# Optimization experiments

Hardware: AMD Instinct MI355X
Metric: run time of the kernel (lower is better)

Reference implementation:

```python
import jax, jax.numpy as jnp
import numpy as np

N_NODES = 100000
N_EDGES = 4800000


def gcn_conv(x, edge_index, W, b):
    """PyG GCNConv: add self-loops, symmetric deg^-1/2 normalization, scatter-add."""
    n = x.shape[0]
    loops = jnp.arange(n, dtype=edge_index.dtype)
    src = jnp.concatenate([edge_index[0], loops])  # [E+N] message sources
    dst = jnp.concatenate([edge_index[1], loops])  # [E+N] message targets
    deg = jax.ops.segment_sum(jnp.ones_like(dst, dtype=x.dtype), dst, num_segments=n)
    dinv = jnp.where(deg > 0, jax.lax.rsqrt(deg), 0.0)  # deg^{-1/2}, guard isolated nodes
    norm = dinv[src] * dinv[dst]                  # [E+N]
    h = x @ W                                      # [N, out] tiny GEMM
    msg = h[src] * norm[:, None]                   # gather + scale (memory bound)
    out = jax.ops.segment_sum(msg, dst, num_segments=n)  # scatter-add
    return out + b


def setup_inputs() -> dict:
    key = jax.random.key(0)
    k1, k2, k3, k4 = jax.random.split(key, 4)
    node_features = jax.random.normal(k1, (N_NODES, 1), dtype=jnp.float32)
    edge_index = jax.random.randint(k2, (2, N_EDGES), 0, N_NODES, dtype=jnp.int32)
    W1 = jax.random.normal(k3, (1, 16), dtype=jnp.float32) / jnp.sqrt(1.0)
    b1 = jnp.zeros((16,), dtype=jnp.float32)
    W2 = jax.random.normal(k4, (16, 2), dtype=jnp.float32) / jnp.sqrt(16.0)
    b2 = jnp.zeros((2,), dtype=jnp.float32)
    return {"node_features": node_features, "edge_index": edge_index,
            "W1": W1, "b1": b1, "W2": W2, "b2": b2}


def reference(node_features, edge_index, W1, b1, W2, b2):
    h = gcn_conv(node_features, edge_index, W1, b1)
    h = jax.nn.relu(h)
    h = gcn_conv(h, edge_index, W2, b2)
    return jax.nn.log_softmax(h, axis=1)
```

## Files before the change

### kernel.cpp

```cpp
#include <hip/hip_runtime.h>
#include <math.h>


#define NNODES 100000
#define NEDGES 4800000
#define BN 256
#define NB 391
#define NPAD (NB * BN)
#define B1 512
#define CHUNK 9375
#define SEG 4
#define SRC_BITS 17
#define SRC_MASK 0x1FFFF

__global__ __launch_bounds__(512) void hist_k(const int* __restrict__ dst,
                                              int* __restrict__ blockhist, int E) {
    __shared__ int h[NB];
    int blk = blockIdx.x;
    for (int i = threadIdx.x; i < NB; i += 512) h[i] = 0;
    __syncthreads();
    int lo = blk * CHUNK, hi = lo + CHUNK; if (hi > E) hi = E;
    for (int i = lo + threadIdx.x; i < hi; i += 512) atomicAdd(&h[dst[i] >> 8], 1);
    __syncthreads();
    int* row = blockhist + (size_t)blk * NB;
    for (int i = threadIdx.x; i < NB; i += 512) row[i] = h[i];
}

__global__ __launch_bounds__(512) void scanblk_k(const int* __restrict__ blockhist,
                                                 int* __restrict__ offs,
                                                 int* __restrict__ colsum) {
    int b = blockIdx.x, t = threadIdx.x;
    int v = blockhist[(size_t)t * NB + b];
    __shared__ int ps[512];
    ps[t] = v; __syncthreads();
    for (int off = 1; off < 512; off <<= 1) {
        int add = (t >= off) ? ps[t - off] : 0;
        __syncthreads();
        ps[t] += add;
        __syncthreads();
    }
    offs[(size_t)t * NB + b] = ps[t] - v;
    if (t == 511) colsum[b] = ps[t];
}

__global__ __launch_bounds__(512) void base_k(const int* __restrict__ colsum,
                                              int* __restrict__ bucketbase) {
    __shared__ int ps[512];
    int t = threadIdx.x;
    int v = (t < NB) ? colsum[t] : 0;
    ps[t] = v; __syncthreads();
    for (int off = 1; off < 512; off <<= 1) {
        int add = (t >= off) ? ps[t - off] : 0;
        __syncthreads();
        ps[t] += add;
        __syncthreads();
    }
    if (t < NB) bucketbase[t] = ps[t] - v;
}

__global__ __launch_bounds__(512) void binfill_k(const int* __restrict__ src,
                                                 const int* __restrict__ dst,
                                                 const int* __restrict__ offs,
                                                 const int* __restrict__ bucketbase,
                                                 unsigned* __restrict__ recs, int E) {
    __shared__ int cur[NB];
    int blk = blockIdx.x;
    const int* row = offs + (size_t)blk * NB;
    for (int i = threadIdx.x; i < NB; i += 512) cur[i] = bucketbase[i] + row[i];
    __syncthreads();
    int lo = blk * CHUNK, hi = lo + CHUNK; if (hi > E) hi = E;
    for (int i = lo + threadIdx.x; i < hi; i += 512) {
        int d = dst[i];
        int b = d >> 8;
        int pos = atomicAdd(&cur[b], 1);
        recs[pos] = (unsigned)src[i] | ((unsigned)(d & (BN - 1)) << SRC_BITS);
    }
}

__global__ __launch_bounds__(512) void deg_s_k(const unsigned* __restrict__ recs,
                                               const int* __restrict__ bucketbase,
                                               const int* __restrict__ colsum,
                                               int* __restrict__ dpart) {
    int blk = blockIdx.x;
    int b = blk >> 2, sg = blk & (SEG - 1);
    __shared__ int hh[BN];
    if (threadIdx.x < BN) hh[threadIdx.x] = 0;
    __syncthreads();
    int base = bucketbase[b], cnt = colsum[b];
    int lo = base + (int)((long long)cnt * sg / SEG);
    int hi = base + (int)((long long)cnt * (sg + 1) / SEG);
    for (int i = lo + threadIdx.x; i < hi; i += 512)
        atomicAdd(&hh[recs[i] >> SRC_BITS], 1);
    __syncthreads();
    if (threadIdx.x < BN)
        dpart[(size_t)sg * NPAD + b * BN + threadIdx.x] = hh[threadIdx.x];
}

__global__ __launch_bounds__(512) void deg_c_k(const float* __restrict__ x,
                                               const int* __restrict__ dpart,
                                               float* __restrict__ dinv,
                                               float* __restrict__ p, int N) {
    int n = blockIdx.x * blockDim.x + threadIdx.x;
    if (n < N) {
        int d = dpart[n] + dpart[NPAD + n] + dpart[2 * NPAD + n] + dpart[3 * NPAD + n];
        float di = rsqrtf((float)(d + 1));
        dinv[n] = di;
        p[n] = x[n] * di;
    }
}

__global__ __launch_bounds__(512) void agg1_s_k(const unsigned* __restrict__ recs,
                                                const int* __restrict__ bucketbase,
                                                const int* __restrict__ colsum,
                                                const float* __restrict__ p,
                                                float* __restrict__ a1part) {
    int blk = blockIdx.x;
    int b = blk >> 2, sg = blk & (SEG - 1);
    __shared__ float acc[BN];
    if (threadIdx.x < BN) acc[threadIdx.x] = 0.f;
    __syncthreads();
    int base = bucketbase[b], cnt = colsum[b];
    int lo = base + (int)((long long)cnt * sg / SEG);
    int hi = base + (int)((long long)cnt * (sg + 1) / SEG);
    for (int i = lo + threadIdx.x; i < hi; i += 512) {
        unsigned r = recs[i];
        atomicAdd(&acc[r >> SRC_BITS], p[r & SRC_MASK]);
    }
    __syncthreads();
    if (threadIdx.x < BN)
        a1part[(size_t)sg * NPAD + b * BN + threadIdx.x] = acc[threadIdx.x];
}

__global__ __launch_bounds__(512) void agg1_c_k(const float* __restrict__ dinv,
                                                const float* __restrict__ p,
                                                const float* __restrict__ a1part,
                                                const float* __restrict__ W1,
                                                const float* __restrict__ b1,
                                                const float* __restrict__ W2,
                                                float2* __restrict__ g, int N) {
    int n = blockIdx.x * blockDim.x + threadIdx.x;
    if (n < N) {
        float sum = a1part[n] + a1part[NPAD + n] + a1part[2 * NPAD + n] + a1part[3 * NPAD + n];
        float di = dinv[n];
        float s = di * (p[n] + sum);
        float g0 = 0.f, g1 = 0.f;
        #pragma unroll
        for (int k = 0; k < 16; ++k) {
            float h = fmaxf(fmaf(W1[k], s, b1[k]), 0.f);
            g0 = fmaf(h, W2[2 * k + 0], g0);
            g1 = fmaf(h, W2[2 * k + 1], g1);
        }
        g[n] = make_float2(g0 * di, g1 * di);
    }
}

__global__ __launch_bounds__(512) void agg2_s_k(const unsigned* __restrict__ recs,
                                                const int* __restrict__ bucketbase,
                                                const int* __restrict__ colsum,
                                                const float2* __restrict__ g,
                                                float2* __restrict__ a2part) {
    int blk = blockIdx.x;
    int b = blk >> 2, sg = blk & (SEG - 1);
    __shared__ float a0[BN], a1[BN];
    if (threadIdx.x < BN) { a0[threadIdx.x] = 0.f; a1[threadIdx.x] = 0.f; }
    __syncthreads();
    int base = bucketbase[b], cnt = colsum[b];
    int lo = base + (int)((long long)cnt * sg / SEG);
    int hi = base + (int)((long long)cnt * (sg + 1) / SEG);
    for (int i = lo + threadIdx.x; i < hi; i += 512) {
        unsigned r = recs[i];
        float2 gv = g[r & SRC_MASK];
        int li = r >> SRC_BITS;
        atomicAdd(&a0[li], gv.x);
        atomicAdd(&a1[li], gv.y);
    }
    __syncthreads();
    if (threadIdx.x < BN)
        a2part[(size_t)sg * NPAD + b * BN + threadIdx.x] =
            make_float2(a0[threadIdx.x], a1[threadIdx.x]);
}

__global__ __launch_bounds__(512) void agg2_c_k(const float* __restrict__ dinv,
                                                const float2* __restrict__ g,
                                                const float2* __restrict__ a2part,
                                                const float* __restrict__ b2,
                                                float2* __restrict__ out, int N) {
    int n = blockIdx.x * blockDim.x + threadIdx.x;
    if (n < N) {
        float2 q0 = a2part[n], q1 = a2part[NPAD + n];
        float2 q2 = a2part[2 * NPAD + n], q3 = a2part[3 * NPAD + n];
        float s0 = q0.x + q1.x + q2.x + q3.x;
        float s1 = q0.y + q1.y + q2.y + q3.y;
        float di = dinv[n];
        float2 gv = g[n];
        float o0 = fmaf(di, gv.x + s0, b2[0]);
        float o1 = fmaf(di, gv.y + s1, b2[1]);
        float m = fmaxf(o0, o1);
        float lse = m + logf(expf(o0 - m) + expf(o1 - m));
        out[n] = make_float2(o0 - lse, o1 - lse);
    }
}


__global__ void count_deg_k(const int* __restrict__ dst, int* __restrict__ degi, int E) {
    int i = blockIdx.x * blockDim.x + threadIdx.x;
    if (i < E) atomicAdd(&degi[dst[i]], 1);
}
__global__ void node1_k(const float* __restrict__ x, const int* __restrict__ degi,
                        float* __restrict__ dinv, float* __restrict__ p, int N) {
    int n = blockIdx.x * blockDim.x + threadIdx.x;
    if (n < N) {
        float di = rsqrtf((float)(degi[n] + 1));
        dinv[n] = di;
        p[n] = x[n] * di;
    }
}
__global__ void scatter1_k(const int* __restrict__ src, const int* __restrict__ dst,
                           const float* __restrict__ p, float* __restrict__ acc1, int E) {
    int i = blockIdx.x * blockDim.x + threadIdx.x;
    if (i < E) atomicAdd(&acc1[dst[i]], p[src[i]]);
}
__global__ void node2_k(const float* __restrict__ dinv, const float* __restrict__ p,
                        const float* __restrict__ acc1, const float* __restrict__ W1,
                        const float* __restrict__ b1, const float* __restrict__ W2,
                        float2* __restrict__ g, int N) {
    int n = blockIdx.x * blockDim.x + threadIdx.x;
    if (n < N) {
        float di = dinv[n];
        float s = di * (p[n] + acc1[n]);
        float g0 = 0.f, g1 = 0.f;
        #pragma unroll
        for (int k = 0; k < 16; ++k) {
            float h = fmaxf(fmaf(W1[k], s, b1[k]), 0.f);
            g0 = fmaf(h, W2[2 * k + 0], g0);
            g1 = fmaf(h, W2[2 * k + 1], g1);
        }
        g[n] = make_float2(g0 * di, g1 * di);
    }
}
__global__ void scatter2_k(const int* __restrict__ src, const int* __restrict__ dst,
                           const float2* __restrict__ g, float* __restrict__ acc2, int E) {
    int i = blockIdx.x * blockDim.x + threadIdx.x;
    if (i < E) {
        float2 gv = g[src[i]];
        int d = dst[i];
        atomicAdd(&acc2[2 * d + 0], gv.x);
        atomicAdd(&acc2[2 * d + 1], gv.y);
    }
}
__global__ void final_k(const float* __restrict__ dinv, const float2* __restrict__ g,
                        const float2* __restrict__ acc2, const float* __restrict__ b2,
                        float2* __restrict__ out, int N) {
    int n = blockIdx.x * blockDim.x + threadIdx.x;
    if (n < N) {
        float di = dinv[n];
        float2 gv = g[n];
        float2 av = acc2[n];
        float o0 = fmaf(di, gv.x + av.x, b2[0]);
        float o1 = fmaf(di, gv.y + av.y, b2[1]);
        float m = fmaxf(o0, o1);
        float lse = m + logf(expf(o0 - m) + expf(o1 - m));
        out[n] = make_float2(o0 - lse, o1 - lse);
    }
}

extern "C" void kernel_launch(void* const* d_in, const int* in_sizes, int n_in,
                              void* d_out, int out_size, void* d_ws, size_t ws_size,
                              hipStream_t stream) {
    const float* x  = (const float*)d_in[0];
    const int*   ei = (const int*)d_in[1];
    const float* W1 = (const float*)d_in[2];
    const float* b1 = (const float*)d_in[3];
    const float* W2 = (const float*)d_in[4];
    const float* b2 = (const float*)d_in[5];
    float2* out = (float2*)d_out;

    const int N = in_sizes[0];
    const int E = in_sizes[1] / 2;
    const int* src = ei;
    const int* dst = ei + E;

    size_t o_recs = 0;
    size_t o_bh   = o_recs + ((size_t)E * 4 + 255 & ~255UL);
    size_t o_offs = o_bh   + ((size_t)B1 * NB * 4 + 255 & ~255UL);
    size_t o_cs   = o_offs + ((size_t)B1 * NB * 4 + 255 & ~255UL);
    size_t o_bb   = o_cs   + ((size_t)NB * 4 + 255 & ~255UL);
    size_t o_dinv = o_bb   + ((size_t)NB * 4 + 255 & ~255UL);
    size_t o_p    = o_dinv + ((size_t)N * 4 + 255 & ~255UL);
    size_t o_g    = o_p    + ((size_t)N * 4 + 255 & ~255UL);
    size_t o_dp   = o_g    + ((size_t)N * 8 + 255 & ~255UL);
    size_t o_a1p  = o_dp   + ((size_t)SEG * NPAD * 4 + 255 & ~255UL);
    size_t o_a2p  = o_a1p  + ((size_t)SEG * NPAD * 4 + 255 & ~255UL);
    size_t need   = o_a2p  + (size_t)SEG * NPAD * 8;

    if (N == NNODES && E == NEDGES && ws_size >= need) {
        char* ws = (char*)d_ws;
        unsigned* recs = (unsigned*)(ws + o_recs);
        int* blockhist = (int*)(ws + o_bh);
        int* offs      = (int*)(ws + o_offs);
        int* colsum    = (int*)(ws + o_cs);
        int* bucketbase= (int*)(ws + o_bb);
        float* dinv    = (float*)(ws + o_dinv);
        float* p       = (float*)(ws + o_p);
        float2* g      = (float2*)(ws + o_g);
        int* dpart     = (int*)(ws + o_dp);
        float* a1part  = (float*)(ws + o_a1p);
        float2* a2part = (float2*)(ws + o_a2p);

        const int gN = (N + 511) / 512;
        hist_k   <<<B1, 512, 0, stream>>>(dst, blockhist, E);
        scanblk_k<<<NB, 512, 0, stream>>>(blockhist, offs, colsum);
        base_k   <<<1, 512, 0, stream>>>(colsum, bucketbase);
        binfill_k<<<B1, 512, 0, stream>>>(src, dst, offs, bucketbase, recs, E);
        deg_s_k  <<<NB * SEG, 512, 0, stream>>>(recs, bucketbase, colsum, dpart);
        deg_c_k  <<<gN, 512, 0, stream>>>(x, dpart, dinv, p, N);
        agg1_s_k <<<NB * SEG, 512, 0, stream>>>(recs, bucketbase, colsum, p, a1part);
        agg1_c_k <<<gN, 512, 0, stream>>>(dinv, p, a1part, W1, b1, W2, g, N);
        agg2_s_k <<<NB * SEG, 512, 0, stream>>>(recs, bucketbase, colsum, g, a2part);
        agg2_c_k <<<gN, 512, 0, stream>>>(dinv, g, a2part, b2, out, N);
    } else {
        char* ws = (char*)d_ws;
        int*    degi = (int*)(ws);
        float*  acc1 = (float*)(ws + 4UL * N);
        float*  acc2 = (float*)(ws + 8UL * N);
        float*  dinvf= (float*)(ws + 16UL * N);
        float*  pf   = (float*)(ws + 20UL * N);
        float2* gf   = (float2*)(ws + 24UL * N);
        const int B = 256;
        const int gE = (E + B - 1) / B;
        const int gNf = (N + B - 1) / B;
        hipMemsetAsync(ws, 0, 16UL * N, stream);
        count_deg_k<<<gE, B, 0, stream>>>(dst, degi, E);
        node1_k<<<gNf, B, 0, stream>>>(x, degi, dinvf, pf, N);
        scatter1_k<<<gE, B, 0, stream>>>(src, dst, pf, acc1, E);
        node2_k<<<gNf, B, 0, stream>>>(dinvf, pf, acc1, W1, b1, W2, gf, N);
        scatter2_k<<<gE, B, 0, stream>>>(src, dst, gf, acc2, E);
        final_k<<<gNf, B, 0, stream>>>(dinvf, gf, (const float2*)acc2, b2, out, N);
    }
}
```

Before: 238.4 us.

## Stage binfill records in shared memory and write them out coalesced per bucket

The binning kernel now does a local scan of its per-block histogram and first scatters each record into a shared-memory buffer grouped by bucket. It then writes the buffer to the global record array in order, finding each element's bucket by binary search over the local prefix sums. Consecutive threads therefore write contiguous runs within each bucket instead of random global addresses. The cost is about 40KB of shared memory per block, an extra scan and binary search per element, and possibly lower occupancy.

```diff
diff --git a/kernel.cpp b/kernel.cpp
--- a/kernel.cpp
+++ b/kernel.cpp
@@ -60,20 +60,52 @@
 
 __global__ __launch_bounds__(512) void binfill_k(const int* __restrict__ src,
                                                  const int* __restrict__ dst,
+                                                 const int* __restrict__ blockhist,
                                                  const int* __restrict__ offs,
                                                  const int* __restrict__ bucketbase,
                                                  unsigned* __restrict__ recs, int E) {
-    __shared__ int cur[NB];
-    int blk = blockIdx.x;
-    const int* row = offs + (size_t)blk * NB;
-    for (int i = threadIdx.x; i < NB; i += 512) cur[i] = bucketbase[i] + row[i];
-    __syncthreads();
+    __shared__ int ps[512];
+    __shared__ int ls[NB + 1];
+    __shared__ int ggap[NB];
+    __shared__ int lcur[NB];
+    __shared__ unsigned lrec[CHUNK];
+    int blk = blockIdx.x, t = threadIdx.x;
+
+    int c = (t < NB) ? blockhist[(size_t)blk * NB + t] : 0;
+    ps[t] = c; __syncthreads();
+    for (int off = 1; off < 512; off <<= 1) {
+        int add = (t >= off) ? ps[t - off] : 0;
+        __syncthreads();
+        ps[t] += add;
+        __syncthreads();
+    }
+    if (t == 0) ls[0] = 0;
+    if (t < NB) ls[t + 1] = ps[t];
+    __syncthreads();
+    if (t < NB) {
+        int lst = ls[t];
+        lcur[t] = lst;
+        ggap[t] = bucketbase[t] + offs[(size_t)blk * NB + t] - lst;
+    }
+    __syncthreads();
+
     int lo = blk * CHUNK, hi = lo + CHUNK; if (hi > E) hi = E;
-    for (int i = lo + threadIdx.x; i < hi; i += 512) {
+    for (int i = lo + t; i < hi; i += 512) {
         int d = dst[i];
         int b = d >> 8;
-        int pos = atomicAdd(&cur[b], 1);
-        recs[pos] = (unsigned)src[i] | ((unsigned)(d & (BN - 1)) << SRC_BITS);
+        int lp = atomicAdd(&lcur[b], 1);
+        lrec[lp] = (unsigned)src[i] | ((unsigned)(d & (BN - 1)) << SRC_BITS);
+    }
+    __syncthreads();
+
+    int cl = hi - lo;
+    for (int j = t; j < cl; j += 512) {
+        int lo2 = 0, hi2 = NB;
+        while (hi2 - lo2 > 1) {
+            int mid = (lo2 + hi2) >> 1;
+            if (ls[mid] <= j) lo2 = mid; else hi2 = mid;
+        }
+        recs[ggap[lo2] + j] = lrec[j];
     }
 }
 
@@ -311,7 +343,7 @@
         hist_k   <<<B1, 512, 0, stream>>>(dst, blockhist, E);
         scanblk_k<<<NB, 512, 0, stream>>>(blockhist, offs, colsum);
         base_k   <<<1, 512, 0, stream>>>(colsum, bucketbase);
-        binfill_k<<<B1, 512, 0, stream>>>(src, dst, offs, bucketbase, recs, E);
+        binfill_k<<<B1, 512, 0, stream>>>(src, dst, blockhist, offs, bucketbase, recs, E);
         deg_s_k  <<<NB * SEG, 512, 0, stream>>>(recs, bucketbase, colsum, dpart);
         deg_c_k  <<<gN, 512, 0, stream>>>(x, dpart, dinv, p, N);
         agg1_s_k <<<NB * SEG, 512, 0, stream>>>(recs, bucketbase, colsum, p, a1part);
```

Result: faster. 228.0 us (-4.3%).
